# Kernel optimization log

Hardware: AMD Instinct MI355X
Metric: run time of the kernel (lower is better)

Reference implementation:

```python
import jax, jax.numpy as jnp
import numpy as np

B, L, D = 8, 2048, 256
D_MODEL = 1024
NUM_SIGNALS = 16
MAX_POSITIONS = 4096
ROLE_OUTPUT = 2  # role id used for the CLS token


def setup_inputs() -> dict:
    key = jax.random.key(0)
    ks = jax.random.split(key, 12)
    emb = jax.random.normal(ks[0], (B, L, D), dtype=jnp.float32)
    pos = jax.random.randint(ks[1], (B, L), 1, MAX_POSITIONS + 1)          # pos >= 1 for real tokens
    sid = jax.random.randint(ks[2], (B, L), 0, NUM_SIGNALS)
    role = jax.random.randint(ks[3], (B, L), 0, 3)
    padding_mask = jax.random.uniform(ks[4], (B, L)) < 0.75                # True = real token
    # learned parameters
    proj_W = jax.random.normal(ks[5], (NUM_SIGNALS, D_MODEL, D), dtype=jnp.float32) * (1.0 / np.sqrt(D))
    proj_b = jax.random.normal(ks[6], (NUM_SIGNALS, D_MODEL), dtype=jnp.float32) * 0.01
    cls_content = jax.random.normal(ks[7], (D_MODEL,), dtype=jnp.float32)
    pos_embed = jax.random.normal(ks[8], (MAX_POSITIONS + 1, D_MODEL), dtype=jnp.float32)
    id_embed = jax.random.normal(ks[9], (NUM_SIGNALS + 1, D_MODEL), dtype=jnp.float32)
    role_embed = jax.random.normal(ks[10], (3, D_MODEL), dtype=jnp.float32)
    return dict(emb=emb, pos=pos, sid=sid, role=role, padding_mask=padding_mask,
                proj_W=proj_W, proj_b=proj_b, cls_content=cls_content,
                pos_embed=pos_embed, id_embed=id_embed, role_embed=role_embed)


def reference(emb, pos, sid, role, padding_mask,
              proj_W, proj_b, cls_content, pos_embed, id_embed, role_embed):
    Bv, Lv, _ = emb.shape
    S, d_model, _ = proj_W.shape
    cls_id = S

    # Grouped per-signal projection: one GEMM per signal id, select per token.
    tokens = jnp.zeros((Bv, Lv, d_model), dtype=emb.dtype)
    for s in range(S):
        proj_s = jnp.einsum('bld,ed->ble', emb, proj_W[s]) + proj_b[s]   # (B, L, d_model)
        keep = ((sid == s) & padding_mask)[..., None]
        tokens = jnp.where(keep, proj_s, tokens)

    # Prepend CLS
    cls = jnp.broadcast_to(cls_content[None, None, :], (Bv, 1, d_model))
    tokens = jnp.concatenate([cls, tokens], axis=1)                       # (B, L+1, d_model)

    pos_full = jnp.concatenate([jnp.zeros((Bv, 1), dtype=pos.dtype), pos], axis=1)
    sid_full = jnp.concatenate([jnp.full((Bv, 1), cls_id, dtype=sid.dtype), sid], axis=1)
    role_full = jnp.concatenate([jnp.full((Bv, 1), ROLE_OUTPUT, dtype=role.dtype), role], axis=1)

    tokens = tokens + pos_embed[pos_full] + id_embed[sid_full] + role_embed[role_full]

    attn_keep = jnp.concatenate([jnp.ones((Bv, 1), dtype=bool), padding_mask], axis=1)
    return tokens, attn_keep
```

## Files before the change

kernel.cpp:

```cpp
#include <hip/hip_runtime.h>
#include <hip/hip_bf16.h>
#include <stdint.h>

#define B_ 8
#define L_ 2048
#define NTOK 16384
#define DK 256
#define DM 1024
#define NS 16
#define LOUT 2049
#define TOK_OUT (B_*LOUT*DM)
#define ATTN_OUT (B_*LOUT)
#define PCAP 2048

typedef unsigned short u16;
typedef unsigned int u32;
typedef __bf16 bf16x8 __attribute__((ext_vector_type(8)));
typedef float f32x4 __attribute__((ext_vector_type(4)));

__device__ inline float bf2f(u16 u) {
    u32 x = ((u32)u) << 16;
    float f;
    __builtin_memcpy(&f, &x, 4);
    return f;
}

__device__ inline u32 packbf2(float lo, float hi) {
    u32 a, b;
    __builtin_memcpy(&a, &lo, 4);
    __builtin_memcpy(&b, &hi, 4);
    a = (a + 0x8000u) >> 16;
    b = (b + 0x8000u) & 0xFFFF0000u;
    return a | b;
}

__device__ inline void gll16(const void* g, void* l) {
    __builtin_amdgcn_global_load_lds(
        (const __attribute__((address_space(1))) unsigned int*)g,
        (__attribute__((address_space(3))) unsigned int*)l, 16, 0, 0);
}

#define WS_CUR 0
#define WS_PERM 64
#define WS_MASK (64 + NS * PCAP)
#define A_OFF 262144ULL
#define APAD_ROWS 18432
#define W_OFF (A_OFF + (unsigned long long)APAD_ROWS * 512ULL)
#define PE_OFF (W_OFF + 16384ULL * 512ULL)
#define WS_NEED (PE_OFF + 4097ULL * 1024ULL * 2ULL)

__global__ __launch_bounds__(256) void sort_kernel(const unsigned char* __restrict__ mb,
                                                   const int* __restrict__ sid,
                                                   int* __restrict__ wsi) {
    __shared__ int f_c1ge2, f_ge2, f_odd;
    __shared__ int lcnt[NS], gbase[NS];
    int tid = threadIdx.x;
    if (tid == 0) { f_c1ge2 = 0; f_ge2 = 0; f_odd = 0; }
    if (tid < NS) lcnt[tid] = 0;
    __syncthreads();

    int c1ge2 = 0, ge2 = 0, oddnz = 0;
    const u32* mw = (const u32*)mb;
    #pragma unroll
    for (int i = 0; i < 16; i++) {
        u32 x = mw[tid * 16 + i];
        u32 b0 = x & 0xFF, b1 = (x >> 8) & 0xFF, b2 = (x >> 16) & 0xFF, b3 = x >> 24;
        if (b1 >= 2) c1ge2 = 1;
        if (b0 >= 2 || b1 >= 2 || b2 >= 2 || b3 >= 2) ge2 = 1;
        if ((b1 | b3) != 0) oddnz = 1;
    }
    if (c1ge2) atomicOr(&f_c1ge2, 1);
    if (ge2) atomicOr(&f_ge2, 1);
    if (oddnz) atomicOr(&f_odd, 1);
    __syncthreads();

    int width;
    if (f_c1ge2) width = 2;
    else if (f_ge2) width = 4;
    else if (f_odd) width = 1;
    else width = 4;

    int t = blockIdx.x * 256 + tid;
    int m;
    if (width == 1) m = (mb[t] != 0);
    else if (width == 2) m = (((const u16*)mb)[t] != 0);
    else m = (((const u32*)mb)[t] != 0);

    wsi[WS_MASK + t] = m;
    int s = sid[t];
    int lr = 0;
    if (m) lr = atomicAdd(&lcnt[s], 1);
    __syncthreads();
    if (tid < NS) gbase[tid] = atomicAdd(&wsi[WS_CUR + tid], lcnt[tid]);
    __syncthreads();
    if (m) {
        int r = gbase[s] + lr;
        if (r < PCAP) wsi[WS_PERM + s * PCAP + r] = t;
    }
}

__global__ __launch_bounds__(256) void prep_kernel(const float* __restrict__ emb,
                                                   const float* __restrict__ W,
                                                   const float* __restrict__ pos_emb,
                                                   const int* __restrict__ wsi,
                                                   unsigned char* __restrict__ wsb) {
    int bid = blockIdx.x;
    int tid = threadIdx.x;
    int lane = tid & 63;
    int wv = tid >> 6;
    if (bid < 4608) {
        int cnts[NS], segoff[NS];
        int accp = 0;
        #pragma unroll
        for (int i = 0; i < NS; i++) {
            int c = wsi[WS_CUR + i];
            cnts[i] = c > PCAP ? PCAP : c;
            segoff[i] = accp;
            accp += ((cnts[i] + 127) >> 7) << 7;
        }
        int r = bid * 4 + wv;
        if (r >= accp) return;
        int s = 0;
        #pragma unroll
        for (int i = 1; i < NS; i++) if (r >= segoff[i]) s = i;
        int local = r - segoff[s];
        u16* Ab = (u16*)(wsb + A_OFF);
        uint2 o;
        if (local < cnts[s]) {
            int t = wsi[WS_PERM + s * PCAP + local];
            float4 a = *(const float4*)(emb + (size_t)t * DK + lane * 4);
            o.x = packbf2(a.x, a.y);
            o.y = packbf2(a.z, a.w);
        } else {
            o.x = 0; o.y = 0;
        }
        *(uint2*)(Ab + (size_t)r * DK + lane * 4) = o;
    } else if (bid < 4608 + 4096) {
        int r = (bid - 4608) * 4 + wv;
        u16* Wb = (u16*)(wsb + W_OFF);
        float4 a = *(const float4*)(W + (size_t)r * DK + lane * 4);
        uint2 o;
        o.x = packbf2(a.x, a.y);
        o.y = packbf2(a.z, a.w);
        *(uint2*)(Wb + (size_t)r * DK + lane * 4) = o;
    } else {
        int r = bid - (4608 + 4096);
        u16* Pb = (u16*)(wsb + PE_OFF);
        int c = tid * 4;
        float4 a = *(const float4*)(pos_emb + (size_t)r * DM + c);
        uint2 o;
        o.x = packbf2(a.x, a.y);
        o.y = packbf2(a.z, a.w);
        *(uint2*)(Pb + (size_t)r * DM + c) = o;
    }
}

__global__ __launch_bounds__(512, 4) void gemm_big(
    const int* __restrict__ pos, const int* __restrict__ role,
    const float* __restrict__ bias,
    const float* __restrict__ id_emb, const float* __restrict__ role_emb,
    const int* __restrict__ wsi, const unsigned char* __restrict__ wsb,
    float* __restrict__ out) {
    __shared__ u16 As[2][128 * 32];
    __shared__ u16 Bs[2][256 * 32];
    __shared__ int toks[128];
    int tid = threadIdx.x;
    int lane = tid & 63;
    int wv = tid >> 6;

    int cnts[NS];
    int mtot = 0;
    #pragma unroll
    for (int i = 0; i < NS; i++) {
        int c = wsi[WS_CUR + i];
        cnts[i] = c > PCAP ? PCAP : c;
        mtot += (cnts[i] + 127) >> 7;
    }
    int bi = (int)blockIdx.x;
    int xcd = bi & 7;
    int j = bi >> 3;
    int m_lo = (xcd * mtot) >> 3;
    int m_hi = ((xcd + 1) * mtot) >> 3;
    int cm = m_hi - m_lo;
    if (cm <= 0 || j >= cm * 4) return;
    int nt = j / cm;
    int m = m_lo + (j - nt * cm);
    int n0 = nt << 8;

    int s = -1, lrt = 0, seg0 = 0;
    {
        int accp = 0;
        #pragma unroll
        for (int i = 0; i < NS; i++) {
            int rt = (cnts[i] + 127) >> 7;
            if (s < 0) {
                if (m < rt) { s = i; lrt = m; seg0 = accp; }
                else m -= rt;
            }
            accp += rt << 7;
        }
    }
    if (s < 0) return;
    int rowsValid = cnts[s] - lrt * 128;
    if (rowsValid > 128) rowsValid = 128;

    if (tid < 128) toks[tid] = (tid < rowsValid) ? wsi[WS_PERM + s * PCAP + lrt * 128 + tid] : -1;

    const u16* Ab = (const u16*)(wsb + A_OFF) + (size_t)(seg0 + lrt * 128) * DK;
    const u16* Bb = (const u16*)(wsb + W_OFF) + (size_t)(s * DM + n0) * DK;
    const u16* Pb = (const u16*)(wsb + PE_OFF);

    int srow = lane >> 2;
    int slseg = lane & 3;

    f32x4 acc[4][4];
    #pragma unroll
    for (int im = 0; im < 4; im++)
        #pragma unroll
        for (int jn = 0; jn < 4; jn++) acc[im][jn] = (f32x4){0.f, 0.f, 0.f, 0.f};

    int wm = wv & 1, wn = wv >> 1;
    int mcol = lane & 15;
    int quad = lane >> 4;

#define STAGE(kc, bf)                                                          \
    {                                                                          \
        int arow = wv * 16 + srow;                                             \
        int ags = (slseg - (arow >> 1)) & 3;                                   \
        gll16(Ab + (size_t)arow * DK + (kc) * 32 + ags * 8,                    \
              &As[bf][wv * 16 * 32]);                                          \
        gll16(Bb + (size_t)arow * DK + (kc) * 32 + ags * 8,                    \
              &Bs[bf][wv * 16 * 32]);                                          \
        int brow1 = 128 + arow;                                                \
        int bgs1 = (slseg - (brow1 >> 1)) & 3;                                 \
        gll16(Bb + (size_t)brow1 * DK + (kc) * 32 + bgs1 * 8,                  \
              &Bs[bf][(128 + wv * 16) * 32]);                                  \
    }

    STAGE(0, 0)
    #pragma unroll
    for (int kc = 0; kc < 8; ++kc) {
        __syncthreads();
        if (kc < 7) STAGE(kc + 1, (kc + 1) & 1)
        int bf = kc & 1;
        bf16x8 af[4], bfr[4];
        #pragma unroll
        for (int im = 0; im < 4; im++) {
            int row = wm * 64 + im * 16 + mcol;
            int sg = (quad + (row >> 1)) & 3;
            af[im] = *(const bf16x8*)(&As[bf][row * 32 + sg * 8]);
        }
        #pragma unroll
        for (int jn = 0; jn < 4; jn++) {
            int row = wn * 64 + jn * 16 + mcol;
            int sg = (quad + (row >> 1)) & 3;
            bfr[jn] = *(const bf16x8*)(&Bs[bf][row * 32 + sg * 8]);
        }
        #pragma unroll
        for (int im = 0; im < 4; im++)
            #pragma unroll
            for (int jn = 0; jn < 4; jn++)
                acc[im][jn] = __builtin_amdgcn_mfma_f32_16x16x32_bf16(
                    af[im], bfr[jn], acc[im][jn], 0, 0, 0);
    }

    float bc[4];
    #pragma unroll
    for (int jn = 0; jn < 4; jn++) {
        int col = n0 + wn * 64 + jn * 16 + mcol;
        bc[jn] = bias[s * DM + col] + id_emb[s * DM + col];
    }
    #pragma unroll
    for (int im = 0; im < 4; im++) {
        #pragma unroll
        for (int r = 0; r < 4; r++) {
            int rowT = wm * 64 + im * 16 + quad * 4 + r;
            if (rowT >= rowsValid) continue;
            int t = toks[rowT];
            int p = pos[t];
            int ro = role[t];
            int b = t >> 11, l = t & 2047;
            size_t orow = (size_t)(b * LOUT + l + 1) * DM;
            const u16* prow = Pb + (size_t)p * DM;
            #pragma unroll
            for (int jn = 0; jn < 4; jn++) {
                int col = n0 + wn * 64 + jn * 16 + mcol;
                float val = acc[im][jn][r] + bc[jn]
                    + bf2f(prow[col])
                    + role_emb[ro * DM + col];
                out[orow + col] = val;
            }
        }
    }
#undef STAGE
}

__global__ __launch_bounds__(256) void ew_kernel(
    const int* __restrict__ pos, const int* __restrict__ sid,
    const int* __restrict__ role,
    const float* __restrict__ cls, const float* __restrict__ pos_emb,
    const float* __restrict__ id_emb, const float* __restrict__ role_emb,
    const int* __restrict__ wsi, float* __restrict__ out) {
    int bi = blockIdx.x;
    int tid = threadIdx.x;
    int lane = tid & 63;
    int wv = tid >> 6;
    if (bi < NTOK / 4) {
        int t = bi * 4 + wv;
        if (wsi[WS_MASK + t]) return;
        int p = pos[t], sd = sid[t], ro = role[t];
        int b = t >> 11, l = t & 2047;
        size_t orow = (size_t)(b * LOUT + l + 1) * DM;
        #pragma unroll
        for (int it = 0; it < 4; it++) {
            int c = it * 256 + lane * 4;
            float4 a = *(const float4*)(pos_emb + (size_t)p * DM + c);
            float4 d = *(const float4*)(id_emb + (size_t)sd * DM + c);
            float4 e = *(const float4*)(role_emb + (size_t)ro * DM + c);
            float4 o;
            o.x = a.x + d.x + e.x;
            o.y = a.y + d.y + e.y;
            o.z = a.z + d.z + e.z;
            o.w = a.w + d.w + e.w;
            *(float4*)(out + orow + c) = o;
        }
    } else if (bi < NTOK / 4 + 2) {
        int b = (bi - NTOK / 4) * 4 + wv;
        size_t orow = (size_t)(b * LOUT) * DM;
        #pragma unroll
        for (int it = 0; it < 4; it++) {
            int c = it * 256 + lane * 4;
            float4 cc = *(const float4*)(cls + c);
            float4 a = *(const float4*)(pos_emb + c);
            float4 d = *(const float4*)(id_emb + NS * DM + c);
            float4 e = *(const float4*)(role_emb + 2 * DM + c);
            float4 o;
            o.x = cc.x + a.x + d.x + e.x;
            o.y = cc.y + a.y + d.y + e.y;
            o.z = cc.z + a.z + d.z + e.z;
            o.w = cc.w + a.w + d.w + e.w;
            *(float4*)(out + orow + c) = o;
        }
    } else {
        int i = (bi - NTOK / 4 - 2) * 256 + tid;
        if (i < ATTN_OUT) {
            int b = i / LOUT;
            int j = i - b * LOUT;
            float val = (j == 0) ? 1.0f : (float)wsi[WS_MASK + b * L_ + j - 1];
            out[TOK_OUT + i] = val;
        }
    }
}

extern "C" void kernel_launch(void* const* d_in, const int* in_sizes, int n_in,
                              void* d_out, int out_size, void* d_ws, size_t ws_size,
                              hipStream_t stream) {
    const float* emb = (const float*)d_in[0];
    const int* pos = (const int*)d_in[1];
    const int* sid = (const int*)d_in[2];
    const int* role = (const int*)d_in[3];
    const unsigned char* mask = (const unsigned char*)d_in[4];
    const float* W = (const float*)d_in[5];
    const float* bias = (const float*)d_in[6];
    const float* cls = (const float*)d_in[7];
    const float* pos_emb = (const float*)d_in[8];
    const float* id_emb = (const float*)d_in[9];
    const float* role_emb = (const float*)d_in[10];
    float* out = (float*)d_out;
    int* wsi = (int*)d_ws;
    unsigned char* wsb = (unsigned char*)d_ws;

    hipMemsetAsync(wsi, 0, 64 * sizeof(int), stream);
    hipLaunchKernelGGL(sort_kernel, dim3(64), dim3(256), 0, stream, mask, sid, wsi);
    hipLaunchKernelGGL(prep_kernel, dim3(4608 + 4096 + 4097), dim3(256), 0, stream,
                       emb, W, pos_emb, wsi, wsb);
    hipLaunchKernelGGL(gemm_big, dim3(576), dim3(512), 0, stream,
                       pos, role, bias, id_emb, role_emb, wsi, wsb, out);
    hipLaunchKernelGGL(ew_kernel, dim3(NTOK / 4 + 2 + 65), dim3(256), 0, stream,
                       pos, sid, role, cls, pos_emb, id_emb, role_emb, wsi, out);
}
```

Before: 155.6 us.

## Fuse sort with bf16 conversion and gather GEMM rows directly from emb

Merges the sort and conversion kernels into one launch that converts all emb and W rows to bf16 in token order. The separate permuted, padded A buffer is dropped: the GEMM gathers A rows through the token index list inside its async LDS loads. The elementwise padding and CLS work moves into the GEMM launch as extra blocks, and the bf16 pos_embed copy is replaced by direct fp32 reads. Nontemporal stores are used for output. This cuts two launches and a gather pass, at the cost of scattered A-row loads in the GEMM.

```diff
diff --git a/kernel.cpp b/kernel.cpp
--- a/kernel.cpp
+++ b/kernel.cpp
@@ -43,130 +43,143 @@
 #define WS_CUR 0
 #define WS_PERM 64
 #define WS_MASK (64 + NS * PCAP)
-#define A_OFF 262144ULL
-#define APAD_ROWS 18432
-#define W_OFF (A_OFF + (unsigned long long)APAD_ROWS * 512ULL)
-#define PE_OFF (W_OFF + 16384ULL * 512ULL)
-#define WS_NEED (PE_OFF + 4097ULL * 1024ULL * 2ULL)
-
-__global__ __launch_bounds__(256) void sort_kernel(const unsigned char* __restrict__ mb,
-                                                   const int* __restrict__ sid,
-                                                   int* __restrict__ wsi) {
+#define EMB_OFF 262144ULL
+#define W_OFF (EMB_OFF + 16384ULL * 512ULL)
+#define WS_NEED (W_OFF + 16384ULL * 512ULL)
+
+__global__ __launch_bounds__(256) void prep_all(
+    const unsigned char* __restrict__ mb, const int* __restrict__ sid,
+    const float* __restrict__ emb, const float* __restrict__ W,
+    int* __restrict__ wsi, unsigned char* __restrict__ wsb) {
     __shared__ int f_c1ge2, f_ge2, f_odd;
     __shared__ int lcnt[NS], gbase[NS];
-    int tid = threadIdx.x;
-    if (tid == 0) { f_c1ge2 = 0; f_ge2 = 0; f_odd = 0; }
-    if (tid < NS) lcnt[tid] = 0;
-    __syncthreads();
-
-    int c1ge2 = 0, ge2 = 0, oddnz = 0;
-    const u32* mw = (const u32*)mb;
-    #pragma unroll
-    for (int i = 0; i < 16; i++) {
-        u32 x = mw[tid * 16 + i];
-        u32 b0 = x & 0xFF, b1 = (x >> 8) & 0xFF, b2 = (x >> 16) & 0xFF, b3 = x >> 24;
-        if (b1 >= 2) c1ge2 = 1;
-        if (b0 >= 2 || b1 >= 2 || b2 >= 2 || b3 >= 2) ge2 = 1;
-        if ((b1 | b3) != 0) oddnz = 1;
-    }
-    if (c1ge2) atomicOr(&f_c1ge2, 1);
-    if (ge2) atomicOr(&f_ge2, 1);
-    if (oddnz) atomicOr(&f_odd, 1);
-    __syncthreads();
-
-    int width;
-    if (f_c1ge2) width = 2;
-    else if (f_ge2) width = 4;
-    else if (f_odd) width = 1;
-    else width = 4;
-
-    int t = blockIdx.x * 256 + tid;
-    int m;
-    if (width == 1) m = (mb[t] != 0);
-    else if (width == 2) m = (((const u16*)mb)[t] != 0);
-    else m = (((const u32*)mb)[t] != 0);
-
-    wsi[WS_MASK + t] = m;
-    int s = sid[t];
-    int lr = 0;
-    if (m) lr = atomicAdd(&lcnt[s], 1);
-    __syncthreads();
-    if (tid < NS) gbase[tid] = atomicAdd(&wsi[WS_CUR + tid], lcnt[tid]);
-    __syncthreads();
-    if (m) {
-        int r = gbase[s] + lr;
-        if (r < PCAP) wsi[WS_PERM + s * PCAP + r] = t;
-    }
-}
-
-__global__ __launch_bounds__(256) void prep_kernel(const float* __restrict__ emb,
-                                                   const float* __restrict__ W,
-                                                   const float* __restrict__ pos_emb,
-                                                   const int* __restrict__ wsi,
-                                                   unsigned char* __restrict__ wsb) {
     int bid = blockIdx.x;
     int tid = threadIdx.x;
+
+    if (bid < 64) {
+        if (tid == 0) { f_c1ge2 = 0; f_ge2 = 0; f_odd = 0; }
+        if (tid < NS) lcnt[tid] = 0;
+        __syncthreads();
+
+        int c1ge2 = 0, ge2 = 0, oddnz = 0;
+        const u32* mw = (const u32*)mb;
+        #pragma unroll
+        for (int i = 0; i < 16; i++) {
+            u32 x = mw[tid * 16 + i];
+            u32 b0 = x & 0xFF, b1 = (x >> 8) & 0xFF, b2 = (x >> 16) & 0xFF, b3 = x >> 24;
+            if (b1 >= 2) c1ge2 = 1;
+            if (b0 >= 2 || b1 >= 2 || b2 >= 2 || b3 >= 2) ge2 = 1;
+            if ((b1 | b3) != 0) oddnz = 1;
+        }
+        if (c1ge2) atomicOr(&f_c1ge2, 1);
+        if (ge2) atomicOr(&f_ge2, 1);
+        if (oddnz) atomicOr(&f_odd, 1);
+        __syncthreads();
+
+        int width;
+        if (f_c1ge2) width = 2;
+        else if (f_ge2) width = 4;
+        else if (f_odd) width = 1;
+        else width = 4;
+
+        int t = bid * 256 + tid;
+        int m;
+        if (width == 1) m = (mb[t] != 0);
+        else if (width == 2) m = (((const u16*)mb)[t] != 0);
+        else m = (((const u32*)mb)[t] != 0);
+
+        wsi[WS_MASK + t] = m;
+        int s = sid[t];
+        int lr = 0;
+        if (m) lr = atomicAdd(&lcnt[s], 1);
+        __syncthreads();
+        if (tid < NS) gbase[tid] = atomicAdd(&wsi[WS_CUR + tid], lcnt[tid]);
+        __syncthreads();
+        if (m) {
+            int r = gbase[s] + lr;
+            if (r < PCAP) wsi[WS_PERM + s * PCAP + r] = t;
+        }
+        return;
+    }
+
+    int cb = bid - 64;
     int lane = tid & 63;
     int wv = tid >> 6;
-    if (bid < 4608) {
-        int cnts[NS], segoff[NS];
-        int accp = 0;
-        #pragma unroll
-        for (int i = 0; i < NS; i++) {
-            int c = wsi[WS_CUR + i];
-            cnts[i] = c > PCAP ? PCAP : c;
-            segoff[i] = accp;
-            accp += ((cnts[i] + 127) >> 7) << 7;
-        }
-        int r = bid * 4 + wv;
-        if (r >= accp) return;
-        int s = 0;
-        #pragma unroll
-        for (int i = 1; i < NS; i++) if (r >= segoff[i]) s = i;
-        int local = r - segoff[s];
-        u16* Ab = (u16*)(wsb + A_OFF);
-        uint2 o;
-        if (local < cnts[s]) {
-            int t = wsi[WS_PERM + s * PCAP + local];
-            float4 a = *(const float4*)(emb + (size_t)t * DK + lane * 4);
-            o.x = packbf2(a.x, a.y);
-            o.y = packbf2(a.z, a.w);
-        } else {
-            o.x = 0; o.y = 0;
-        }
-        *(uint2*)(Ab + (size_t)r * DK + lane * 4) = o;
-    } else if (bid < 4608 + 4096) {
-        int r = (bid - 4608) * 4 + wv;
-        u16* Wb = (u16*)(wsb + W_OFF);
-        float4 a = *(const float4*)(W + (size_t)r * DK + lane * 4);
-        uint2 o;
-        o.x = packbf2(a.x, a.y);
-        o.y = packbf2(a.z, a.w);
-        *(uint2*)(Wb + (size_t)r * DK + lane * 4) = o;
+    const float* src;
+    u16* dst;
+    if (cb < 4096) {
+        src = emb;
+        dst = (u16*)(wsb + EMB_OFF);
     } else {
-        int r = bid - (4608 + 4096);
-        u16* Pb = (u16*)(wsb + PE_OFF);
-        int c = tid * 4;
-        float4 a = *(const float4*)(pos_emb + (size_t)r * DM + c);
-        uint2 o;
-        o.x = packbf2(a.x, a.y);
-        o.y = packbf2(a.z, a.w);
-        *(uint2*)(Pb + (size_t)r * DM + c) = o;
-    }
-}
-
-__global__ __launch_bounds__(512, 4) void gemm_big(
-    const int* __restrict__ pos, const int* __restrict__ role,
-    const float* __restrict__ bias,
-    const float* __restrict__ id_emb, const float* __restrict__ role_emb,
+        cb -= 4096;
+        src = W;
+        dst = (u16*)(wsb + W_OFF);
+    }
+    int r = cb * 4 + wv;
+    float4 a = *(const float4*)(src + (size_t)r * DK + lane * 4);
+    uint2 o;
+    o.x = packbf2(a.x, a.y);
+    o.y = packbf2(a.z, a.w);
+    *(uint2*)(dst + (size_t)r * DK + lane * 4) = o;
+}
+
+__global__ __launch_bounds__(512, 4) void fused_main(
+    const int* __restrict__ pos, const int* __restrict__ sid,
+    const int* __restrict__ role,
+    const float* __restrict__ bias, const float* __restrict__ cls,
+    const float* __restrict__ pos_emb, const float* __restrict__ id_emb,
+    const float* __restrict__ role_emb,
     const int* __restrict__ wsi, const unsigned char* __restrict__ wsb,
     float* __restrict__ out) {
     __shared__ u16 As[2][128 * 32];
     __shared__ u16 Bs[2][256 * 32];
     __shared__ int toks[128];
+    int bi = (int)blockIdx.x;
     int tid = threadIdx.x;
     int lane = tid & 63;
     int wv = tid >> 6;
+
+    if (bi >= 576) {
+        int eb = bi - 576;
+        if (eb < NTOK / 8) {
+            int t = eb * 8 + wv;
+            if (wsi[WS_MASK + t]) return;
+            int p = pos[t], sd = sid[t], ro = role[t];
+            int b = t >> 11, l = t & 2047;
+            size_t orow = (size_t)(b * LOUT + l + 1) * DM;
+            #pragma unroll
+            for (int it = 0; it < 4; it++) {
+                int c = it * 256 + lane * 4;
+                f32x4 a = *(const f32x4*)(pos_emb + (size_t)p * DM + c);
+                f32x4 d = *(const f32x4*)(id_emb + (size_t)sd * DM + c);
+                f32x4 e = *(const f32x4*)(role_emb + (size_t)ro * DM + c);
+                f32x4 o = a + d + e;
+                __builtin_nontemporal_store(o, (f32x4*)(out + orow + c));
+            }
+        } else if (eb == NTOK / 8) {
+            int b = wv;
+            size_t orow = (size_t)(b * LOUT) * DM;
+            #pragma unroll
+            for (int it = 0; it < 4; it++) {
+                int c = it * 256 + lane * 4;
+                f32x4 cc = *(const f32x4*)(cls + c);
+                f32x4 a = *(const f32x4*)(pos_emb + c);
+                f32x4 d = *(const f32x4*)(id_emb + NS * DM + c);
+                f32x4 e = *(const f32x4*)(role_emb + 2 * DM + c);
+                f32x4 o = cc + a + d + e;
+                *(f32x4*)(out + orow + c) = o;
+            }
+        } else {
+            int i = (eb - NTOK / 8 - 1) * 512 + tid;
+            if (i < ATTN_OUT) {
+                int b = i / LOUT;
+                int j = i - b * LOUT;
+                float val = (j == 0) ? 1.0f : (float)wsi[WS_MASK + b * L_ + j - 1];
+                out[TOK_OUT + i] = val;
+            }
+        }
+        return;
+    }
 
     int cnts[NS];
     int mtot = 0;
@@ -176,7 +189,6 @@
         cnts[i] = c > PCAP ? PCAP : c;
         mtot += (cnts[i] + 127) >> 7;
     }
-    int bi = (int)blockIdx.x;
     int xcd = bi & 7;
     int j = bi >> 3;
     int m_lo = (xcd * mtot) >> 3;
@@ -187,31 +199,35 @@
     int m = m_lo + (j - nt * cm);
     int n0 = nt << 8;
 
-    int s = -1, lrt = 0, seg0 = 0;
-    {
-        int accp = 0;
-        #pragma unroll
-        for (int i = 0; i < NS; i++) {
-            int rt = (cnts[i] + 127) >> 7;
-            if (s < 0) {
-                if (m < rt) { s = i; lrt = m; seg0 = accp; }
-                else m -= rt;
-            }
-            accp += rt << 7;
+    int s = -1, lrt = 0;
+    #pragma unroll
+    for (int i = 0; i < NS; i++) {
+        int rt = (cnts[i] + 127) >> 7;
+        if (s < 0) {
+            if (m < rt) { s = i; lrt = m; }
+            else m -= rt;
         }
     }
     if (s < 0) return;
     int rowsValid = cnts[s] - lrt * 128;
     if (rowsValid > 128) rowsValid = 128;
 
-    if (tid < 128) toks[tid] = (tid < rowsValid) ? wsi[WS_PERM + s * PCAP + lrt * 128 + tid] : -1;
-
-    const u16* Ab = (const u16*)(wsb + A_OFF) + (size_t)(seg0 + lrt * 128) * DK;
+    if (tid < 128) {
+        int base = WS_PERM + s * PCAP + lrt * 128;
+        toks[tid] = wsi[base + ((tid < rowsValid) ? tid : 0)];
+    }
+    __syncthreads();
+
+    const u16* Eb = (const u16*)(wsb + EMB_OFF);
     const u16* Bb = (const u16*)(wsb + W_OFF) + (size_t)(s * DM + n0) * DK;
-    const u16* Pb = (const u16*)(wsb + PE_OFF);
 
     int srow = lane >> 2;
     int slseg = lane & 3;
+    int arow = wv * 16 + srow;
+    int ags = (slseg - (arow >> 1)) & 3;
+    int brow1 = 128 + arow;
+    int bgs1 = (slseg - (brow1 >> 1)) & 3;
+    const u16* Asrc = Eb + (size_t)toks[arow] * DK;
 
     f32x4 acc[4][4];
     #pragma unroll
@@ -225,14 +241,9 @@
 
 #define STAGE(kc, bf)                                                          \
     {                                                                          \
-        int arow = wv * 16 + srow;                                             \
-        int ags = (slseg - (arow >> 1)) & 3;                                   \
-        gll16(Ab + (size_t)arow * DK + (kc) * 32 + ags * 8,                    \
-              &As[bf][wv * 16 * 32]);                                          \
+        gll16(Asrc + (kc) * 32 + ags * 8, &As[bf][wv * 16 * 32]);              \
         gll16(Bb + (size_t)arow * DK + (kc) * 32 + ags * 8,                    \
               &Bs[bf][wv * 16 * 32]);                                          \
-        int brow1 = 128 + arow;                                                \
-        int bgs1 = (slseg - (brow1 >> 1)) & 3;                                 \
         gll16(Bb + (size_t)brow1 * DK + (kc) * 32 + bgs1 * 8,                  \
               &Bs[bf][(128 + wv * 16) * 32]);                                  \
     }
@@ -281,75 +292,18 @@
             int ro = role[t];
             int b = t >> 11, l = t & 2047;
             size_t orow = (size_t)(b * LOUT + l + 1) * DM;
-            const u16* prow = Pb + (size_t)p * DM;
+            const float* prow = pos_emb + (size_t)p * DM;
             #pragma unroll
             for (int jn = 0; jn < 4; jn++) {
                 int col = n0 + wn * 64 + jn * 16 + mcol;
                 float val = acc[im][jn][r] + bc[jn]
-                    + bf2f(prow[col])
+                    + prow[col]
                     + role_emb[ro * DM + col];
-                out[orow + col] = val;
+                __builtin_nontemporal_store(val, &out[orow + col]);
             }
         }
     }
 #undef STAGE
-}
-
-__global__ __launch_bounds__(256) void ew_kernel(
-    const int* __restrict__ pos, const int* __restrict__ sid,
-    const int* __restrict__ role,
-    const float* __restrict__ cls, const float* __restrict__ pos_emb,
-    const float* __restrict__ id_emb, const float* __restrict__ role_emb,
-    const int* __restrict__ wsi, float* __restrict__ out) {
-    int bi = blockIdx.x;
-    int tid = threadIdx.x;
-    int lane = tid & 63;
-    int wv = tid >> 6;
-    if (bi < NTOK / 4) {
-        int t = bi * 4 + wv;
-        if (wsi[WS_MASK + t]) return;
-        int p = pos[t], sd = sid[t], ro = role[t];
-        int b = t >> 11, l = t & 2047;
-        size_t orow = (size_t)(b * LOUT + l + 1) * DM;
-        #pragma unroll
-        for (int it = 0; it < 4; it++) {
-            int c = it * 256 + lane * 4;
-            float4 a = *(const float4*)(pos_emb + (size_t)p * DM + c);
-            float4 d = *(const float4*)(id_emb + (size_t)sd * DM + c);
-            float4 e = *(const float4*)(role_emb + (size_t)ro * DM + c);
-            float4 o;
-            o.x = a.x + d.x + e.x;
-            o.y = a.y + d.y + e.y;
-            o.z = a.z + d.z + e.z;
-            o.w = a.w + d.w + e.w;
-            *(float4*)(out + orow + c) = o;
-        }
-    } else if (bi < NTOK / 4 + 2) {
-        int b = (bi - NTOK / 4) * 4 + wv;
-        size_t orow = (size_t)(b * LOUT) * DM;
-        #pragma unroll
-        for (int it = 0; it < 4; it++) {
-            int c = it * 256 + lane * 4;
-            float4 cc = *(const float4*)(cls + c);
-            float4 a = *(const float4*)(pos_emb + c);
-            float4 d = *(const float4*)(id_emb + NS * DM + c);
-            float4 e = *(const float4*)(role_emb + 2 * DM + c);
-            float4 o;
-            o.x = cc.x + a.x + d.x + e.x;
-            o.y = cc.y + a.y + d.y + e.y;
-            o.z = cc.z + a.z + d.z + e.z;
-            o.w = cc.w + a.w + d.w + e.w;
-            *(float4*)(out + orow + c) = o;
-        }
-    } else {
-        int i = (bi - NTOK / 4 - 2) * 256 + tid;
-        if (i < ATTN_OUT) {
-            int b = i / LOUT;
-            int j = i - b * LOUT;
-            float val = (j == 0) ? 1.0f : (float)wsi[WS_MASK + b * L_ + j - 1];
-            out[TOK_OUT + i] = val;
-        }
-    }
 }
 
 extern "C" void kernel_launch(void* const* d_in, const int* in_sizes, int n_in,
@@ -370,12 +324,10 @@
     int* wsi = (int*)d_ws;
     unsigned char* wsb = (unsigned char*)d_ws;
 
-    hipMemsetAsync(wsi, 0, 64 * sizeof(int), stream);
-    hipLaunchKernelGGL(sort_kernel, dim3(64), dim3(256), 0, stream, mask, sid, wsi);
-    hipLaunchKernelGGL(prep_kernel, dim3(4608 + 4096 + 4097), dim3(256), 0, stream,
-                       emb, W, pos_emb, wsi, wsb);
-    hipLaunchKernelGGL(gemm_big, dim3(576), dim3(512), 0, stream,
-                       pos, role, bias, id_emb, role_emb, wsi, wsb, out);
-    hipLaunchKernelGGL(ew_kernel, dim3(NTOK / 4 + 2 + 65), dim3(256), 0, stream,
-                       pos, sid, role, cls, pos_emb, id_emb, role_emb, wsi, out);
-}
+    (void)hipMemsetAsync(wsi, 0, 64 * sizeof(int), stream);
+    hipLaunchKernelGGL(prep_all, dim3(64 + 8192), dim3(256), 0, stream,
+                       mask, sid, emb, W, wsi, wsb);
+    hipLaunchKernelGGL(fused_main, dim3(576 + 2048 + 1 + 33), dim3(512), 0, stream,
+                       pos, sid, role, bias, cls, pos_emb, id_emb, role_emb,
+                       wsi, wsb, out);
+}
```

New measurement: 154.1 us. Within noise of the previous version (-1.0%).
